# Optimization experiments

Hardware: AMD Instinct MI355X
Metric: run time of the kernel (lower is better)

The kernel has to match this reference:

```python
import jax, jax.numpy as jnp
import numpy as np


def _cdist(x, y):
    # Euclidean (L2) distance matrix, matching torch.cdist default p=2.
    # x: [B,N,D], y: [B,M,D] -> [B,N,M]
    x2 = jnp.sum(x * x, axis=-1, keepdims=True)          # [B,N,1]
    y2 = jnp.sum(y * y, axis=-1, keepdims=True)          # [B,M,1]
    d2 = x2 + jnp.swapaxes(y2, -1, -2) - 2.0 * jnp.einsum('bnd,bmd->bnm', x, y)
    return jnp.sqrt(jnp.maximum(d2, 0.0))


def setup_inputs() -> dict:
    key = jax.random.key(0)
    k1, k2, k3 = jax.random.split(key, 3)
    B, N, G, D = 1, 8192, 2048, 64
    expression = jax.random.normal(k1, (B, N, G), dtype=jnp.float32)
    encoding = jax.random.normal(k2, (B, N, D), dtype=jnp.float32)
    quality = jax.random.normal(k3, (B, N, 1), dtype=jnp.float32)
    return {"expression": expression, "encoding": encoding, "quality": quality}


def reference(expression, encoding, quality):
    # scores[b,i,j] = -||enc_i - enc_j|| + quality[b,j]
    scores = -_cdist(encoding, encoding) + jnp.swapaxes(quality, -1, -2)  # [B,N,N]
    similarity = jax.nn.softmax(scores, axis=-1)
    return similarity @ expression  # [B,N,G]
```

## Files before the change

kernel.cpp:

```cpp
#include <hip/hip_runtime.h>
#include <hip/hip_bf16.h>


typedef __attribute__((ext_vector_type(8))) short bf16x8;
typedef __attribute__((ext_vector_type(4))) float f32x4;
typedef __attribute__((ext_vector_type(16))) float f32x16;

constexpr int N_ = 8192;
constexpr int G_ = 2048;
constexpr int D_ = 64;

__device__ __forceinline__ unsigned short f32_to_bf16(float f) {
  unsigned u = __builtin_bit_cast(unsigned, f);
  u = (u + 0x7FFFu + ((u >> 16) & 1u)) >> 16;
  return (unsigned short)u;
}
__device__ __forceinline__ float bf16_to_f32(unsigned short h) {
  unsigned u = ((unsigned)h) << 16;
  return __builtin_bit_cast(float, u);
}

typedef __attribute__((address_space(1))) const unsigned int glob_u32;
typedef __attribute__((address_space(3))) unsigned int lds_u32;
__device__ __forceinline__ void gload_lds16(const void* g, void* l) {
  __builtin_amdgcn_global_load_lds((glob_u32*)g, (lds_u32*)l, 16, 0, 0);
}

__global__ void prep_kernel(const float* __restrict__ enc,
                            const float* __restrict__ quality,
                            float* __restrict__ norms,
                            float2* __restrict__ nq,
                            unsigned short* __restrict__ encb) {
  int row = blockIdx.x * blockDim.x + threadIdx.x;
  if (row >= N_) return;
  const float* r = enc + (size_t)row * D_;
  float n = 0.f;
#pragma unroll
  for (int k = 0; k < D_; k += 4) {
    float4 v = *(const float4*)(r + k);
    n += v.x * v.x + v.y * v.y + v.z * v.z + v.w * v.w;
    ushort4 h;
    h.x = f32_to_bf16(v.x); h.y = f32_to_bf16(v.y);
    h.z = f32_to_bf16(v.z); h.w = f32_to_bf16(v.w);
    *(ushort4*)(encb + (size_t)row * D_ + k) = h;
  }
  norms[row] = n;
  nq[row] = make_float2(n, quality[row]);
}

__global__ void etrans_kernel(const float* __restrict__ E,
                              unsigned short* __restrict__ ET) {
  __shared__ __align__(16) unsigned short t[64 * 72];
  int j0 = blockIdx.x * 64;
  int g0 = blockIdx.y * 64;
  int tid = threadIdx.x;
#pragma unroll
  for (int it = 0; it < 4; ++it) {
    int r = it * 16 + (tid >> 4);
    int c4 = tid & 15;
    float4 v = *(const float4*)(E + (size_t)(j0 + r) * G_ + g0 + c4 * 4);
    t[(c4 * 4 + 0) * 72 + r] = f32_to_bf16(v.x);
    t[(c4 * 4 + 1) * 72 + r] = f32_to_bf16(v.y);
    t[(c4 * 4 + 2) * 72 + r] = f32_to_bf16(v.z);
    t[(c4 * 4 + 3) * 72 + r] = f32_to_bf16(v.w);
  }
  __syncthreads();
#pragma unroll
  for (int it = 0; it < 2; ++it) {
    int g = it * 32 + (tid >> 3);
    int ch = tid & 7;
    bf16x8 v = *(const bf16x8*)(&t[g * 72 + ch * 8]);
    *(bf16x8*)(ET + (size_t)(g0 + g) * N_ + j0 + ch * 8) = v;
  }
}

__global__ __launch_bounds__(256)
void pk_kernel(const unsigned short* __restrict__ encb,
               const float* __restrict__ norms,
               const float2* __restrict__ nq,
               unsigned short* __restrict__ P,
               float* __restrict__ lpart) {
  __shared__ __align__(16) unsigned short p_lds[64 * 72];

  const int tid = threadIdx.x;
  const int wave = tid >> 6;
  const int lane = tid & 63;
  const int quad = lane >> 4;
  const int l15 = lane & 15;

  const int i0 = blockIdx.y * 64;
  const int jbase = blockIdx.x * 1024;
  const int irow_a = i0 + 16 * wave + l15;
  const int iloc_c = 16 * wave + quad * 4;
  const int irow_c = i0 + iloc_c;

  const int srow_loc = 16 * wave + (lane >> 2);

  bf16x8 afrag[2];
#pragma unroll
  for (int ks = 0; ks < 2; ++ks)
    afrag[ks] = *(const bf16x8*)(encb + (size_t)irow_a * 64 + ks * 32 + quad * 8);

  float ni[4];
#pragma unroll
  for (int r = 0; r < 4; ++r) ni[r] = norms[irow_c + r];

  float lsum[4] = {0.f, 0.f, 0.f, 0.f};

  for (int js = 0; js < 16; ++js) {
    const int j0j = jbase + js * 64;
#pragma unroll
    for (int jt = 0; jt < 4; ++jt) {
      const int jrow = j0j + jt * 16 + l15;
      bf16x8 b0 = *(const bf16x8*)(encb + (size_t)jrow * 64 + quad * 8);
      bf16x8 b1 = *(const bf16x8*)(encb + (size_t)jrow * 64 + 32 + quad * 8);
      float2 njq = nq[jrow];
      f32x4 s4 = {0.f, 0.f, 0.f, 0.f};
      s4 = __builtin_amdgcn_mfma_f32_16x16x32_bf16(afrag[0], b0, s4, 0, 0, 0);
      s4 = __builtin_amdgcn_mfma_f32_16x16x32_bf16(afrag[1], b1, s4, 0, 0, 0);
#pragma unroll
      for (int r = 0; r < 4; ++r) {
        float d2 = fmaxf(ni[r] + njq.x - 2.0f * s4[r], 0.f);
        float sc = njq.y - sqrtf(d2);
        if (irow_c + r == jrow) sc = njq.y;
        float p = __expf(sc);
        unsigned short pb = f32_to_bf16(p);
        lsum[r] += bf16_to_f32(pb);
        p_lds[(iloc_c + r) * 72 + jt * 16 + l15] = pb;
      }
    }
    __syncthreads();
#pragma unroll
    for (int k = 0; k < 2; ++k) {
      int c = (lane & 3) + k * 4;
      bf16x8 v = *(const bf16x8*)(&p_lds[srow_loc * 72 + c * 8]);
      *(bf16x8*)(P + (size_t)(i0 + srow_loc) * N_ + j0j + c * 8) = v;
    }
    __syncthreads();
  }
#pragma unroll
  for (int r = 0; r < 4; ++r) {
    float v = lsum[r];
    v += __shfl_xor(v, 1);
    v += __shfl_xor(v, 2);
    v += __shfl_xor(v, 4);
    v += __shfl_xor(v, 8);
    lsum[r] = v;
  }
  if (l15 == 0) {
#pragma unroll
    for (int r = 0; r < 4; ++r)
      lpart[(size_t)blockIdx.x * N_ + irow_c + r] = lsum[r];
  }
}

__global__ void inv_kernel(const float* __restrict__ lpart,
                           float* __restrict__ linv) {
  int i = blockIdx.x * blockDim.x + threadIdx.x;
  if (i >= N_) return;
  float s = 0.f;
#pragma unroll
  for (int c = 0; c < 8; ++c) s += lpart[(size_t)c * N_ + i];
  linv[i] = 1.0f / s;
}

constexpr int GBM = 256, GBN = 256, GBK = 32;
constexpr int GNT = N_ / GBK;
constexpr int SLOT_A = GBM * GBK;
constexpr int SLOT_B = GBN * GBK;
constexpr int SLOT = SLOT_A + SLOT_B;
constexpr int GEMM_LDS_BYTES = 3 * SLOT * 2;

__global__ __launch_bounds__(512, 2)
void gemm8_kernel(const unsigned short* __restrict__ P,
                  const unsigned short* __restrict__ ET,
                  const float* __restrict__ linv,
                  float* __restrict__ out) {
  extern __shared__ __align__(16) unsigned short smem[];

  const int tid = threadIdx.x;
  const int wave = tid >> 6;
  const int lane = tid & 63;
  const int quad = lane >> 4;
  const int l15 = lane & 15;

  const int bid = blockIdx.x;
  const int lg = (bid & 7) * 32 + (bid >> 3);
  const int gx = lg & 7;
  const int gy = lg >> 3;
  const int g0 = gx * GBN;
  const int i0 = gy * GBM;

  const int wm = wave >> 2;
  const int wn = wave & 3;
  const int wrow = wm * 128;
  const int wcol = wn * 64;

  unsigned short* s0 = smem;
  unsigned short* s1 = smem + SLOT;
  unsigned short* s2 = smem + 2 * SLOT;

  const int strow = tid >> 2;
  const int stch = tid & 3;
  const int csw = stch ^ ((strow >> 1) & 3);
  const int dstA = strow * GBK + stch * 8;
  unsigned gA0 = (unsigned)(i0 + strow) * N_ + csw * 8;
  unsigned gA1 = (unsigned)(i0 + 128 + strow) * N_ + csw * 8;
  unsigned gB0 = (unsigned)(g0 + strow) * N_ + csw * 8;
  unsigned gB1 = (unsigned)(g0 + 128 + strow) * N_ + csw * 8;

  const int fswz = (quad ^ ((l15 >> 1) & 3)) * 8;
  const int aBase = (wrow + l15) * GBK + fswz;
  const int bBase = SLOT_A + (wcol + l15) * GBK + fswz;

  f32x4 acc[8][4];
#pragma unroll
  for (int a = 0; a < 8; ++a)
#pragma unroll
    for (int b = 0; b < 4; ++b) acc[a][b] = (f32x4){0.f, 0.f, 0.f, 0.f};

  bf16x8 fa0[8], fb0[4], fa1[8], fb1[4];

  gload_lds16(P + gA0, s0 + dstA);
  gload_lds16(P + gA1, s0 + dstA + 4096);
  gload_lds16(ET + gB0, s0 + SLOT_A + dstA);
  gload_lds16(ET + gB1, s0 + SLOT_A + dstA + 4096);
  gA0 += GBK; gA1 += GBK; gB0 += GBK; gB1 += GBK;
  gload_lds16(P + gA0, s1 + dstA);
  gload_lds16(P + gA1, s1 + dstA + 4096);
  gload_lds16(ET + gB0, s1 + SLOT_A + dstA);
  gload_lds16(ET + gB1, s1 + SLOT_A + dstA + 4096);
  gA0 += GBK; gA1 += GBK; gB0 += GBK; gB1 += GBK;
  asm volatile("s_waitcnt vmcnt(4)" ::: "memory");
  __builtin_amdgcn_s_barrier();
  {
    const unsigned short* pa = s0 + aBase;
    const unsigned short* pb = s0 + bBase;
#pragma unroll
    for (int r = 0; r < 4; ++r) fb0[r] = *(const bf16x8*)(pb + r * 512);
#pragma unroll
    for (int r = 0; r < 4; ++r) fa0[r] = *(const bf16x8*)(pa + r * 512);
#pragma unroll
    for (int r = 0; r < 4; ++r) fa0[4 + r] = *(const bf16x8*)(pa + 2048 + r * 512);
  }
  gload_lds16(P + gA0, s2 + dstA);
  gload_lds16(P + gA1, s2 + dstA + 4096);
  gload_lds16(ET + gB0, s2 + SLOT_A + dstA);
  gload_lds16(ET + gB1, s2 + SLOT_A + dstA + 4096);
  gA0 += GBK; gA1 += GBK; gB0 += GBK; gB1 += GBK;
  asm volatile("s_waitcnt vmcnt(4)" ::: "memory");
  asm volatile("s_waitcnt lgkmcnt(0)" ::: "memory");
  __builtin_amdgcn_s_barrier();
  __builtin_amdgcn_sched_barrier(0);

  unsigned short* cur = s1;
  unsigned short* nxt = s2;
  unsigned short* stg = s0;

  int u = 0;
  auto body = [&](bf16x8(&faC)[8], bf16x8(&fbC)[4],
                  bf16x8(&faN)[8], bf16x8(&fbN)[4]) {
    if (u < GNT - 3) {
      gload_lds16(P + gA0, stg + dstA);
      gload_lds16(P + gA1, stg + dstA + 4096);
      gload_lds16(ET + gB0, stg + SLOT_A + dstA);
      gload_lds16(ET + gB1, stg + SLOT_A + dstA + 4096);
      gA0 += GBK; gA1 += GBK; gB0 += GBK; gB1 += GBK;
    }
    if (u < GNT - 1) {
      const unsigned short* pa = cur + aBase;
      const unsigned short* pb = cur + bBase;
#pragma unroll
      for (int r = 0; r < 4; ++r) fbN[r] = *(const bf16x8*)(pb + r * 512);
#pragma unroll
      for (int r = 0; r < 4; ++r) faN[r] = *(const bf16x8*)(pa + r * 512);
#pragma unroll
      for (int r = 0; r < 4; ++r) faN[4 + r] = *(const bf16x8*)(pa + 2048 + r * 512);
    }
    __builtin_amdgcn_s_setprio(1);
#pragma unroll
    for (int r = 0; r < 4; ++r)
#pragma unroll
      for (int c = 0; c < 4; ++c)
        acc[r][c] = __builtin_amdgcn_mfma_f32_16x16x32_bf16(faC[r], fbC[c], acc[r][c], 0, 0, 0);
#pragma unroll
    for (int r = 0; r < 4; ++r)
#pragma unroll
      for (int c = 0; c < 4; ++c)
        acc[4 + r][c] = __builtin_amdgcn_mfma_f32_16x16x32_bf16(faC[4 + r], fbC[c], acc[4 + r][c], 0, 0, 0);
    __builtin_amdgcn_s_setprio(0);
    asm volatile("s_waitcnt lgkmcnt(0)" ::: "memory");
    if (u < GNT - 3) {
      asm volatile("s_waitcnt vmcnt(4)" ::: "memory");
    } else {
      asm volatile("s_waitcnt vmcnt(0)" ::: "memory");
    }
    __builtin_amdgcn_s_barrier();
    __builtin_amdgcn_sched_barrier(0);
    unsigned short* t_ = cur; cur = nxt; nxt = stg; stg = t_;
    ++u;
  };

  for (int it = 0; it < GNT / 2; ++it) {
    body(fa0, fb0, fa1, fb1);
    body(fa1, fb1, fa0, fb0);
  }

#pragma unroll
  for (int rt = 0; rt < 8; ++rt) {
    float lir[4];
#pragma unroll
    for (int r = 0; r < 4; ++r)
      lir[r] = linv[i0 + wrow + rt * 16 + quad * 4 + r];
#pragma unroll
    for (int ct = 0; ct < 4; ++ct)
#pragma unroll
      for (int r = 0; r < 4; ++r) {
        int row = wrow + rt * 16 + quad * 4 + r;
        int col = wcol + ct * 16 + l15;
        out[(size_t)(i0 + row) * G_ + g0 + col] = acc[rt][ct][r] * lir[r];
      }
  }
}

__global__ __launch_bounds__(256, 2)
void gemm_kernel(const unsigned short* __restrict__ P,
                 const unsigned short* __restrict__ ET,
                 const float* __restrict__ linv,
                 float* __restrict__ out) {
  __shared__ __align__(16) unsigned short aT[256 * 64];
  __shared__ __align__(16) unsigned short bT[128 * 64];

  const int tid = threadIdx.x;
  const int wave = tid >> 6;
  const int lane = tid & 63;
  const int quad = lane >> 4;
  const int l15 = lane & 15;

  const int g0 = blockIdx.x * 128;
  const int i0 = blockIdx.y * 256;
  const int wrow = (wave >> 1) * 128;
  const int wcol = (wave & 1) * 64;

  const int strow = tid >> 3;
  const int stc = tid & 7;

  f32x4 acc[8][4];
#pragma unroll
  for (int a = 0; a < 8; ++a)
#pragma unroll
    for (int b = 0; b < 4; ++b) acc[a][b] = (f32x4){0.f, 0.f, 0.f, 0.f};

  for (int kk = 0; kk < N_; kk += 64) {
#pragma unroll
    for (int s = 0; s < 8; ++s) {
      int row = s * 32 + strow;
      int csrc = stc ^ (row & 7);
      gload_lds16(P + (size_t)(i0 + row) * N_ + kk + csrc * 8,
                  &aT[row * 64 + stc * 8]);
    }
#pragma unroll
    for (int s = 0; s < 4; ++s) {
      int row = s * 32 + strow;
      int csrc = stc ^ (row & 7);
      gload_lds16(ET + (size_t)(g0 + row) * N_ + kk + csrc * 8,
                  &bT[row * 64 + stc * 8]);
    }
    __syncthreads();
#pragma unroll
    for (int ks = 0; ks < 2; ++ks) {
      const int swzk = ((ks * 4 + quad) ^ (l15 & 7)) * 8;
      bf16x8 bF[4];
#pragma unroll
      for (int ct = 0; ct < 4; ++ct)
        bF[ct] = *(const bf16x8*)(&bT[(wcol + ct * 16 + l15) * 64 + swzk]);
#pragma unroll
      for (int rt = 0; rt < 8; ++rt) {
        bf16x8 aF = *(const bf16x8*)(&aT[(wrow + rt * 16 + l15) * 64 + swzk]);
#pragma unroll
        for (int ct = 0; ct < 4; ++ct)
          acc[rt][ct] = __builtin_amdgcn_mfma_f32_16x16x32_bf16(aF, bF[ct], acc[rt][ct], 0, 0, 0);
      }
    }
    __syncthreads();
  }

#pragma unroll
  for (int rt = 0; rt < 8; ++rt) {
    float lir[4];
#pragma unroll
    for (int r = 0; r < 4; ++r)
      lir[r] = linv[i0 + wrow + rt * 16 + quad * 4 + r];
#pragma unroll
    for (int ct = 0; ct < 4; ++ct)
#pragma unroll
      for (int r = 0; r < 4; ++r) {
        int row = wrow + rt * 16 + quad * 4 + r;
        int col = wcol + ct * 16 + l15;
        out[(size_t)(i0 + row) * G_ + g0 + col] = acc[rt][ct][r] * lir[r];
      }
  }
}

__global__ __launch_bounds__(256, 2)
void fused_kernel(const unsigned short* __restrict__ encb,
                  const float* __restrict__ norms,
                  const float2* __restrict__ nq,
                  const unsigned short* __restrict__ ET,
                  float* __restrict__ out) {
  __shared__ __align__(16) unsigned short p_lds[128 * 72];
  __shared__ __align__(16) unsigned short e_lds[256 * 72];
  __shared__ float linv_lds[128];

  const int tid = threadIdx.x;
  const int wave = tid >> 6;
  const int lane = tid & 63;
  const int quad = lane >> 4;
  const int l15 = lane & 15;
  const int half = lane >> 5;
  const int l31 = lane & 31;

  const int gt = blockIdx.x & 7;
  const int it = blockIdx.x >> 3;
  const int i0 = it * 128;
  const int g0 = gt * 256;

  const int srow = 32 * wave;
  const int wr = wave >> 1, wc = wave & 1;
  const int prow = 64 * wr;
  const int pcol = 128 * wc;

  bf16x8 afrag[2][2];
#pragma unroll
  for (int rt = 0; rt < 2; ++rt)
#pragma unroll
    for (int ks = 0; ks < 2; ++ks)
      afrag[rt][ks] = *(const bf16x8*)(encb +
          (size_t)(i0 + srow + rt * 16 + l15) * 64 + ks * 32 + quad * 8);

  float ni[2][4];
#pragma unroll
  for (int rt = 0; rt < 2; ++rt)
#pragma unroll
    for (int r = 0; r < 4; ++r)
      ni[rt][r] = norms[i0 + srow + rt * 16 + quad * 4 + r];

  float lsum[2][4] = {};
  f32x16 acc[2][4];
#pragma unroll
  for (int a = 0; a < 2; ++a)
#pragma unroll
    for (int b = 0; b < 4; ++b)
#pragma unroll
      for (int e = 0; e < 16; ++e) acc[a][b][e] = 0.f;

  for (int j0j = 0; j0j < N_; j0j += 64) {
#pragma unroll
    for (int s = 0; s < 8; ++s) {
      int g = s * 32 + (tid >> 3);
      int ch = tid & 7;
      bf16x8 v = *(const bf16x8*)(ET + (size_t)(g0 + g) * N_ + j0j + ch * 8);
      *(bf16x8*)(&e_lds[g * 72 + ch * 8]) = v;
    }
#pragma unroll
    for (int jt = 0; jt < 4; ++jt) {
      const int jrow = j0j + jt * 16 + l15;
      bf16x8 b0 = *(const bf16x8*)(encb + (size_t)jrow * 64 + quad * 8);
      bf16x8 b1 = *(const bf16x8*)(encb + (size_t)jrow * 64 + 32 + quad * 8);
      float2 njq = nq[jrow];
#pragma unroll
      for (int rt = 0; rt < 2; ++rt) {
        f32x4 s4 = {0.f, 0.f, 0.f, 0.f};
        s4 = __builtin_amdgcn_mfma_f32_16x16x32_bf16(afrag[rt][0], b0, s4, 0, 0, 0);
        s4 = __builtin_amdgcn_mfma_f32_16x16x32_bf16(afrag[rt][1], b1, s4, 0, 0, 0);
#pragma unroll
        for (int r = 0; r < 4; ++r) {
          int i_loc = srow + rt * 16 + quad * 4 + r;
          float d2 = fmaxf(ni[rt][r] + njq.x - 2.0f * s4[r], 0.f);
          float sc = njq.y - sqrtf(d2);
          if (i0 + i_loc == jrow) sc = njq.y;
          float p = __expf(sc);
          unsigned short pb = f32_to_bf16(p);
          lsum[rt][r] += bf16_to_f32(pb);
          p_lds[i_loc * 72 + jt * 16 + l15] = pb;
        }
      }
    }
    __syncthreads();
#pragma unroll
    for (int ks = 0; ks < 4; ++ks) {
      bf16x8 pa0 = *(const bf16x8*)(&p_lds[(prow + l31) * 72 + ks * 16 + half * 8]);
      bf16x8 pa1 = *(const bf16x8*)(&p_lds[(prow + 32 + l31) * 72 + ks * 16 + half * 8]);
#pragma unroll
      for (int ct = 0; ct < 4; ++ct) {
        bf16x8 eb = *(const bf16x8*)(&e_lds[(pcol + ct * 32 + l31) * 72 + ks * 16 + half * 8]);
        acc[0][ct] = __builtin_amdgcn_mfma_f32_32x32x16_bf16(pa0, eb, acc[0][ct], 0, 0, 0);
        acc[1][ct] = __builtin_amdgcn_mfma_f32_32x32x16_bf16(pa1, eb, acc[1][ct], 0, 0, 0);
      }
    }
    __syncthreads();
  }

#pragma unroll
  for (int rt = 0; rt < 2; ++rt)
#pragma unroll
    for (int r = 0; r < 4; ++r) {
      float v = lsum[rt][r];
      v += __shfl_xor(v, 1);
      v += __shfl_xor(v, 2);
      v += __shfl_xor(v, 4);
      v += __shfl_xor(v, 8);
      lsum[rt][r] = v;
    }
  if (l15 == 0) {
#pragma unroll
    for (int rt = 0; rt < 2; ++rt)
#pragma unroll
      for (int r = 0; r < 4; ++r)
        linv_lds[srow + rt * 16 + quad * 4 + r] = 1.0f / lsum[rt][r];
  }
  __syncthreads();

#pragma unroll
  for (int rt2 = 0; rt2 < 2; ++rt2)
#pragma unroll
    for (int ct = 0; ct < 4; ++ct)
#pragma unroll
      for (int e = 0; e < 16; ++e) {
        int row = prow + rt2 * 32 + (e & 3) + 8 * (e >> 2) + 4 * half;
        int col = pcol + ct * 32 + l31;
        out[(size_t)(i0 + row) * G_ + g0 + col] = acc[rt2][ct][e] * linv_lds[row];
      }
}

extern "C" void kernel_launch(void* const* d_in, const int* in_sizes, int n_in,
                              void* d_out, int out_size, void* d_ws, size_t ws_size,
                              hipStream_t stream) {
  const float* expr = (const float*)d_in[0];
  const float* enc  = (const float*)d_in[1];
  const float* qual = (const float*)d_in[2];
  float* out = (float*)d_out;

  char* ws = (char*)d_ws;
  const size_t off_norms = 0;
  const size_t off_nq    = 32768;
  const size_t off_lpart = 98304;
  const size_t off_linv  = 360448;
  const size_t off_encb  = 393216;
  const size_t off_ET    = 1441792;
  const size_t off_P     = 34996224;
  const size_t need      = off_P + (size_t)N_ * N_ * 2;

  static bool smem_init = false;
  static bool smem_ok = false;
  if (!smem_init) {
    smem_init = true;
    hipError_t e = hipFuncSetAttribute(
        reinterpret_cast<const void*>(gemm8_kernel),
        hipFuncAttributeMaxDynamicSharedMemorySize, GEMM_LDS_BYTES);
    smem_ok = (e == hipSuccess);
  }

  if (ws_size >= need) {
    float* norms         = (float*)(ws + off_norms);
    float2* nqp          = (float2*)(ws + off_nq);
    float* lpart         = (float*)(ws + off_lpart);
    float* linv          = (float*)(ws + off_linv);
    unsigned short* encb = (unsigned short*)(ws + off_encb);
    unsigned short* ET   = (unsigned short*)(ws + off_ET);
    unsigned short* P    = (unsigned short*)(ws + off_P);

    prep_kernel<<<dim3(N_ / 256), dim3(256), 0, stream>>>(enc, qual, norms, nqp, encb);
    etrans_kernel<<<dim3(N_ / 64, G_ / 64), dim3(256), 0, stream>>>(expr, ET);
    pk_kernel<<<dim3(8, N_ / 64), dim3(256), 0, stream>>>(encb, norms, nqp, P, lpart);
    inv_kernel<<<dim3(N_ / 256), dim3(256), 0, stream>>>(lpart, linv);
    if (smem_ok) {
      gemm8_kernel<<<dim3((N_ / GBM) * (G_ / GBN)), dim3(512), GEMM_LDS_BYTES, stream>>>(
          P, ET, linv, out);
    } else {
      gemm_kernel<<<dim3(G_ / 128, N_ / 256), dim3(256), 0, stream>>>(P, ET, linv, out);
    }
  } else {
    float* norms         = (float*)ws;
    float2* nqp          = (float2*)(ws + 32768);
    unsigned short* encb = (unsigned short*)(ws + 98304);
    unsigned short* ET   = (unsigned short*)(ws + 1146880);
    prep_kernel<<<dim3(N_ / 256), dim3(256), 0, stream>>>(enc, qual, norms, nqp, encb);
    etrans_kernel<<<dim3(N_ / 64, G_ / 64), dim3(256), 0, stream>>>(expr, ET);
    fused_kernel<<<dim3((N_ / 128) * (G_ / 256)), dim3(256), 0, stream>>>(encb, norms, nqp, ET, out);
  }
}
```

Baseline: 411.4 us.

## Load GEMM B fragments directly from global into registers, bypassing LDS

The B operand (ET) of the P·E GEMM is no longer staged through the triple-buffered LDS ring. Each wave now loads its own B fragments straight from global memory into registers one K-step ahead, and the LDS footprint shrinks to the A tiles only. The aim is to cut LDS traffic, LDS capacity and ds_read work for B. In exchange, waves that share a column block load the same B data twice. The per-lane loads are strided across rows, so coalescing is weaker, and only one step of prefetch is left to hide global latency.

```diff
diff --git a/kernel.cpp b/kernel.cpp
--- a/kernel.cpp
+++ b/kernel.cpp
@@ -167,9 +167,7 @@
 constexpr int GBM = 256, GBN = 256, GBK = 32;
 constexpr int GNT = N_ / GBK;
 constexpr int SLOT_A = GBM * GBK;
-constexpr int SLOT_B = GBN * GBK;
-constexpr int SLOT = SLOT_A + SLOT_B;
-constexpr int GEMM_LDS_BYTES = 3 * SLOT * 2;
+constexpr int GEMM_LDS_BYTES = 3 * SLOT_A * 2;
 
 __global__ __launch_bounds__(512, 2)
 void gemm8_kernel(const unsigned short* __restrict__ P,
@@ -197,8 +195,8 @@
   const int wcol = wn * 64;
 
   unsigned short* s0 = smem;
-  unsigned short* s1 = smem + SLOT;
-  unsigned short* s2 = smem + 2 * SLOT;
+  unsigned short* s1 = smem + SLOT_A;
+  unsigned short* s2 = smem + 2 * SLOT_A;
 
   const int strow = tid >> 2;
   const int stch = tid & 3;
@@ -206,12 +204,14 @@
   const int dstA = strow * GBK + stch * 8;
   unsigned gA0 = (unsigned)(i0 + strow) * N_ + csw * 8;
   unsigned gA1 = (unsigned)(i0 + 128 + strow) * N_ + csw * 8;
-  unsigned gB0 = (unsigned)(g0 + strow) * N_ + csw * 8;
-  unsigned gB1 = (unsigned)(g0 + 128 + strow) * N_ + csw * 8;
 
   const int fswz = (quad ^ ((l15 >> 1) & 3)) * 8;
   const int aBase = (wrow + l15) * GBK + fswz;
-  const int bBase = SLOT_A + (wcol + l15) * GBK + fswz;
+
+  unsigned gBf0 = (unsigned)(g0 + wcol + 0 * 16 + l15) * N_ + quad * 8;
+  unsigned gBf1 = (unsigned)(g0 + wcol + 1 * 16 + l15) * N_ + quad * 8;
+  unsigned gBf2 = (unsigned)(g0 + wcol + 2 * 16 + l15) * N_ + quad * 8;
+  unsigned gBf3 = (unsigned)(g0 + wcol + 3 * 16 + l15) * N_ + quad * 8;
 
   f32x4 acc[8][4];
 #pragma unroll
@@ -221,23 +221,21 @@
 
   bf16x8 fa0[8], fb0[4], fa1[8], fb1[4];
 
+  fb0[0] = *(const bf16x8*)(ET + gBf0);
+  fb0[1] = *(const bf16x8*)(ET + gBf1);
+  fb0[2] = *(const bf16x8*)(ET + gBf2);
+  fb0[3] = *(const bf16x8*)(ET + gBf3);
+  gBf0 += GBK; gBf1 += GBK; gBf2 += GBK; gBf3 += GBK;
   gload_lds16(P + gA0, s0 + dstA);
   gload_lds16(P + gA1, s0 + dstA + 4096);
-  gload_lds16(ET + gB0, s0 + SLOT_A + dstA);
-  gload_lds16(ET + gB1, s0 + SLOT_A + dstA + 4096);
-  gA0 += GBK; gA1 += GBK; gB0 += GBK; gB1 += GBK;
+  gA0 += GBK; gA1 += GBK;
   gload_lds16(P + gA0, s1 + dstA);
   gload_lds16(P + gA1, s1 + dstA + 4096);
-  gload_lds16(ET + gB0, s1 + SLOT_A + dstA);
-  gload_lds16(ET + gB1, s1 + SLOT_A + dstA + 4096);
-  gA0 += GBK; gA1 += GBK; gB0 += GBK; gB1 += GBK;
-  asm volatile("s_waitcnt vmcnt(4)" ::: "memory");
+  gA0 += GBK; gA1 += GBK;
+  asm volatile("s_waitcnt vmcnt(2)" ::: "memory");
   __builtin_amdgcn_s_barrier();
   {
     const unsigned short* pa = s0 + aBase;
-    const unsigned short* pb = s0 + bBase;
-#pragma unroll
-    for (int r = 0; r < 4; ++r) fb0[r] = *(const bf16x8*)(pb + r * 512);
 #pragma unroll
     for (int r = 0; r < 4; ++r) fa0[r] = *(const bf16x8*)(pa + r * 512);
 #pragma unroll
@@ -245,11 +243,9 @@
   }
   gload_lds16(P + gA0, s2 + dstA);
   gload_lds16(P + gA1, s2 + dstA + 4096);
-  gload_lds16(ET + gB0, s2 + SLOT_A + dstA);
-  gload_lds16(ET + gB1, s2 + SLOT_A + dstA + 4096);
-  gA0 += GBK; gA1 += GBK; gB0 += GBK; gB1 += GBK;
-  asm volatile("s_waitcnt vmcnt(4)" ::: "memory");
+  gA0 += GBK; gA1 += GBK;
   asm volatile("s_waitcnt lgkmcnt(0)" ::: "memory");
+  asm volatile("s_waitcnt vmcnt(2)" ::: "memory");
   __builtin_amdgcn_s_barrier();
   __builtin_amdgcn_sched_barrier(0);
 
@@ -260,18 +256,20 @@
   int u = 0;
   auto body = [&](bf16x8(&faC)[8], bf16x8(&fbC)[4],
                   bf16x8(&faN)[8], bf16x8(&fbN)[4]) {
+    if (u < GNT - 1) {
+      fbN[0] = *(const bf16x8*)(ET + gBf0);
+      fbN[1] = *(const bf16x8*)(ET + gBf1);
+      fbN[2] = *(const bf16x8*)(ET + gBf2);
+      fbN[3] = *(const bf16x8*)(ET + gBf3);
+      gBf0 += GBK; gBf1 += GBK; gBf2 += GBK; gBf3 += GBK;
+    }
     if (u < GNT - 3) {
       gload_lds16(P + gA0, stg + dstA);
       gload_lds16(P + gA1, stg + dstA + 4096);
-      gload_lds16(ET + gB0, stg + SLOT_A + dstA);
-      gload_lds16(ET + gB1, stg + SLOT_A + dstA + 4096);
-      gA0 += GBK; gA1 += GBK; gB0 += GBK; gB1 += GBK;
+      gA0 += GBK; gA1 += GBK;
     }
     if (u < GNT - 1) {
       const unsigned short* pa = cur + aBase;
-      const unsigned short* pb = cur + bBase;
-#pragma unroll
-      for (int r = 0; r < 4; ++r) fbN[r] = *(const bf16x8*)(pb + r * 512);
 #pragma unroll
       for (int r = 0; r < 4; ++r) faN[r] = *(const bf16x8*)(pa + r * 512);
 #pragma unroll
@@ -291,7 +289,7 @@
     __builtin_amdgcn_s_setprio(0);
     asm volatile("s_waitcnt lgkmcnt(0)" ::: "memory");
     if (u < GNT - 3) {
-      asm volatile("s_waitcnt vmcnt(4)" ::: "memory");
+      asm volatile("s_waitcnt vmcnt(2)" ::: "memory");
     } else {
       asm volatile("s_waitcnt vmcnt(0)" ::: "memory");
     }
```

Result: slower. 540.8 us (+31.4%).
